# Kernel optimization log

Hardware: AMD Instinct MI355X
Metric: run time of the kernel (lower is better)

## Reference

```python
import jax, jax.numpy as jnp
import numpy as np

NUM_SEQS = 64
NUM_HEADS = 32
NUM_KV_HEADS = 8
HEAD_SIZE = 128
BLOCK_SIZE = 16
X = 8  # key cache vector width (16 bytes / fp16 elem size in vLLM)
NUM_BLOCKS = 4096
MAX_BLOCKS_PER_SEQ = 64
MAX_CTX = MAX_BLOCKS_PER_SEQ * BLOCK_SIZE  # 1024
SCALE = 0.08838834764831845  # 1/sqrt(HEAD_SIZE)
Q_PER_KV = NUM_HEADS // NUM_KV_HEADS


def setup_inputs() -> dict:
    key = jax.random.key(0)
    k0, k1, k2, k3, k4 = jax.random.split(key, 5)
    query = jax.random.normal(k0, (NUM_SEQS, NUM_HEADS, HEAD_SIZE), dtype=jnp.float32)
    key_cache = jax.random.normal(
        k1, (NUM_BLOCKS, NUM_KV_HEADS, HEAD_SIZE // X, BLOCK_SIZE, X), dtype=jnp.float32)
    value_cache = jax.random.normal(
        k2, (NUM_BLOCKS, NUM_KV_HEADS, HEAD_SIZE, BLOCK_SIZE), dtype=jnp.float32)
    block_tables = jax.random.randint(
        k3, (NUM_SEQS, MAX_BLOCKS_PER_SEQ), 0, NUM_BLOCKS, dtype=jnp.int32)
    context_lens = jax.random.randint(k4, (NUM_SEQS,), 1, MAX_CTX + 1, dtype=jnp.int32)
    return {"query": query, "key_cache": key_cache, "value_cache": value_cache,
            "block_tables": block_tables, "context_lens": context_lens}


def _paged_attention(query, key_cache, value_cache, block_tables, context_lens):
    nb = key_cache.shape[0]
    # key cache [nb, kvH, hs//x, bs, x] -> [nb, kvH, bs, hs]
    k_tok = jnp.transpose(key_cache, (0, 1, 3, 2, 4)).reshape(nb, NUM_KV_HEADS, BLOCK_SIZE, HEAD_SIZE)
    # value cache [nb, kvH, hs, bs] -> [nb, kvH, bs, hs]
    v_tok = jnp.transpose(value_cache, (0, 1, 3, 2))
    # gather per-sequence paged KV via block tables: [S, MB, kvH, bs, hs] -> [S, MAX_CTX, kvH, hs]
    keys = k_tok[block_tables].transpose(0, 1, 3, 2, 4).reshape(NUM_SEQS, MAX_CTX, NUM_KV_HEADS, HEAD_SIZE)
    values = v_tok[block_tables].transpose(0, 1, 3, 2, 4).reshape(NUM_SEQS, MAX_CTX, NUM_KV_HEADS, HEAD_SIZE)
    # GQA: group query heads over kv heads. q4: [S, kvH, qpkv, hs]
    q4 = query.reshape(NUM_SEQS, NUM_KV_HEADS, Q_PER_KV, HEAD_SIZE)
    # scores: [S, kvH, qpkv, MAX_CTX]
    scores = jnp.einsum('sgqd,skgd->sgqk', q4, keys) * SCALE
    valid = jnp.arange(MAX_CTX, dtype=jnp.int32)[None, :] < context_lens[:, None]  # [S, K]
    scores = jnp.where(valid[:, None, None, :], scores, jnp.float32(-1e30))
    probs = jax.nn.softmax(scores, axis=-1)
    out = jnp.einsum('sgqk,skgd->sgqd', probs, values)
    return out.reshape(NUM_SEQS, NUM_HEADS, HEAD_SIZE)


def reference(query, key_cache, value_cache, block_tables, context_lens):
    return _paged_attention(query, key_cache, value_cache, block_tables, context_lens)
```

## Files before the change

kernel.cpp:

```cpp
#include <hip/hip_runtime.h>

#define NSEQ   64
#define NHEAD  32
#define KVH    8
#define HS     128
#define BS     16
#define MBPS   64
#define MAXCTX 1024
#define QPKV   4
#define SCALE_F 0.08838834764831845f

__launch_bounds__(256)
__global__ void pa_kernel(const float* __restrict__ q,
                          const float* __restrict__ kc,
                          const float* __restrict__ vc,
                          const int*   __restrict__ bt,
                          const int*   __restrict__ cl,
                          float*       __restrict__ out)
{
    const int seq = blockIdx.x >> 3;
    const int kvh = blockIdx.x & 7;
    const int t   = threadIdx.x;
    const int ctx = cl[seq];
    const int nb  = (ctx + BS - 1) / BS;

    __shared__ __align__(16) float sc[QPKV][MAXCTX + 8];
    __shared__ float qs[QPKV][HS];
    __shared__ float l_inv[QPKV];

    for (int i = t; i < QPKV * HS; i += 256) {
        int g = i >> 7, d = i & 127;
        qs[g][d] = q[((size_t)seq * NHEAD + kvh * QPKV + g) * HS + d];
    }
    __syncthreads();

    const int tok   = t >> 4;
    const int dpart = t & 15;
    float qreg[QPKV][8];
#pragma unroll
    for (int g = 0; g < QPKV; ++g)
#pragma unroll
        for (int j = 0; j < 8; ++j)
            qreg[g][j] = qs[g][dpart * 8 + j];

    const int* btrow = bt + seq * MBPS;
    for (int b = 0; b < nb; ++b) {
        const int blk = btrow[b];
        const float* kptr = kc + ((size_t)blk * KVH + kvh) * (HS * BS)
                               + dpart * (BS * 8) + tok * 8;
        const float4 k0 = *(const float4*)kptr;
        const float4 k1 = *(const float4*)(kptr + 4);
        const float kk[8] = {k0.x,k0.y,k0.z,k0.w,k1.x,k1.y,k1.z,k1.w};
        float p[QPKV];
#pragma unroll
        for (int g = 0; g < QPKV; ++g) {
            float s = 0.f;
#pragma unroll
            for (int j = 0; j < 8; ++j) s += qreg[g][j] * kk[j];
            p[g] = s;
        }
#pragma unroll
        for (int off = 8; off >= 1; off >>= 1)
#pragma unroll
            for (int g = 0; g < QPKV; ++g)
                p[g] += __shfl_xor(p[g], off, 16);
        if (dpart < QPKV)
            sc[dpart][b * BS + tok] = p[dpart] * SCALE_F;
    }
    __syncthreads();

    {
        const int w    = t >> 6;
        const int lane = t & 63;
        float m = -1e30f;
        for (int i = lane; i < ctx; i += 64) m = fmaxf(m, sc[w][i]);
#pragma unroll
        for (int off = 32; off >= 1; off >>= 1) m = fmaxf(m, __shfl_xor(m, off));
        float ssum = 0.f;
        const int lim = nb * BS;
        for (int i = lane; i < lim; i += 64) {
            float v = (i < ctx) ? __expf(sc[w][i] - m) : 0.f;
            sc[w][i] = v;
            ssum += v;
        }
#pragma unroll
        for (int off = 32; off >= 1; off >>= 1) ssum += __shfl_xor(ssum, off);
        if (lane == 0) l_inv[w] = 1.f / ssum;
    }
    __syncthreads();

    const int d  = t >> 1;
    const int th = t & 1;
    float acc[QPKV] = {0.f, 0.f, 0.f, 0.f};
    for (int b = 0; b < nb; ++b) {
        const int blk = btrow[b];
        const float* vptr = vc + ((size_t)blk * KVH + kvh) * (HS * BS)
                               + d * BS + th * 8;
        const float4 v0 = *(const float4*)vptr;
        const float4 v1 = *(const float4*)(vptr + 4);
        const float vv[8] = {v0.x,v0.y,v0.z,v0.w,v1.x,v1.y,v1.z,v1.w};
        const int base = b * BS + th * 8;
#pragma unroll
        for (int g = 0; g < QPKV; ++g) {
            const float4 p0 = *(const float4*)&sc[g][base];
            const float4 p1 = *(const float4*)&sc[g][base + 4];
            acc[g] += p0.x*vv[0] + p0.y*vv[1] + p0.z*vv[2] + p0.w*vv[3]
                    + p1.x*vv[4] + p1.y*vv[5] + p1.z*vv[6] + p1.w*vv[7];
        }
    }
#pragma unroll
    for (int g = 0; g < QPKV; ++g)
        acc[g] += __shfl_xor(acc[g], 1);
    if (th == 0) {
#pragma unroll
        for (int g = 0; g < QPKV; ++g)
            out[((size_t)seq * NHEAD + kvh * QPKV + g) * HS + d] = acc[g] * l_inv[g];
    }
}

extern "C" void kernel_launch(void* const* d_in, const int* in_sizes, int n_in,
                              void* d_out, int out_size, void* d_ws, size_t ws_size,
                              hipStream_t stream) {
    const float* query       = (const float*)d_in[0];
    const float* key_cache   = (const float*)d_in[1];
    const float* value_cache = (const float*)d_in[2];
    const int*   block_tables= (const int*)d_in[3];
    const int*   context_lens= (const int*)d_in[4];
    float* out = (float*)d_out;

    dim3 grid(NSEQ * KVH);
    dim3 block(256);
    pa_kernel<<<grid, block, 0, stream>>>(query, key_cache, value_cache,
                                          block_tables, context_lens, out);
}
```

Baseline: 479.2 us.

## Split paged attention over context partitions with a separate combine kernel

Splits each sequence's context into 8 partitions of 128 tokens, one workgroup per partition, and each wave handles one query head of the group. Partial outputs, maxima and sums go to workspace, and a second kernel merges them with a log-sum-exp rescale. The aim is to raise parallelism beyond 512 workgroups and shorten the serial loop over blocks. In exchange it adds a second launch and workspace traffic, and each partition now loads K/V once per query head rather than once for all four.

```diff
diff --git a/kernel.cpp b/kernel.cpp
--- a/kernel.cpp
+++ b/kernel.cpp
@@ -6,130 +6,152 @@
 #define HS     128
 #define BS     16
 #define MBPS   64
-#define MAXCTX 1024
+#define PARTS  8
+#define PSIZE  128
 #define QPKV   4
 #define SCALE_F 0.08838834764831845f
 
-__launch_bounds__(256)
-__global__ void pa_kernel(const float* __restrict__ q,
-                          const float* __restrict__ kc,
-                          const float* __restrict__ vc,
-                          const int*   __restrict__ bt,
-                          const int*   __restrict__ cl,
-                          float*       __restrict__ out)
+#define O_PART_ELEMS (NSEQ*KVH*PARTS*QPKV*HS)
+#define ML_ELEMS     (NSEQ*KVH*PARTS*QPKV)
+
+__launch_bounds__(256, 4)
+__global__ void pa_part(const float* __restrict__ q,
+                        const float* __restrict__ kc,
+                        const float* __restrict__ vc,
+                        const int*   __restrict__ bt,
+                        const int*   __restrict__ cl,
+                        float*       __restrict__ o_part,
+                        float*       __restrict__ m_part,
+                        float*       __restrict__ l_part)
 {
-    const int seq = blockIdx.x >> 3;
-    const int kvh = blockIdx.x & 7;
-    const int t   = threadIdx.x;
-    const int ctx = cl[seq];
-    const int nb  = (ctx + BS - 1) / BS;
+    const int bx   = blockIdx.x;
+    const int part = bx & (PARTS - 1);
+    const int kvh  = (bx >> 3) & (KVH - 1);
+    const int seq  = bx >> 6;
+    const int ctx  = cl[seq];
+    const int tok0 = part * PSIZE;
+    if (tok0 >= ctx) return;
+    const int ntok = min(PSIZE, ctx - tok0);
+    const int nbl  = (ntok + BS - 1) / BS;
 
-    __shared__ __align__(16) float sc[QPKV][MAXCTX + 8];
-    __shared__ float qs[QPKV][HS];
-    __shared__ float l_inv[QPKV];
+    const int w    = threadIdx.x >> 6;
+    const int lane = threadIdx.x & 63;
+    const int tok  = lane & 15;
+    const int dq   = lane >> 4;
 
-    for (int i = t; i < QPKV * HS; i += 256) {
-        int g = i >> 7, d = i & 127;
-        qs[g][d] = q[((size_t)seq * NHEAD + kvh * QPKV + g) * HS + d];
+    __shared__ float sc[QPKV][PSIZE];
+
+    const float* qp = q + ((size_t)seq * NHEAD + kvh * QPKV + w) * HS + dq * 32;
+    float4 qv[8];
+#pragma unroll
+    for (int k = 0; k < 8; ++k) qv[k] = ((const float4*)qp)[k];
+
+    const int* btrow = bt + seq * MBPS + part * (PSIZE / BS);
+
+    for (int b = 0; b < nbl; ++b) {
+        const int blk = btrow[b];
+        const float* kb = kc + ((size_t)blk * KVH + kvh) * (HS * BS);
+        float s = 0.f;
+#pragma unroll
+        for (int k = 0; k < 4; ++k) {
+            const float4* kp = (const float4*)(kb + (dq * 4 + k) * (BS * 8) + tok * 8);
+            const float4 k0 = kp[0], k1 = kp[1];
+            const float4 q0 = qv[2 * k], q1 = qv[2 * k + 1];
+            s += q0.x*k0.x + q0.y*k0.y + q0.z*k0.z + q0.w*k0.w
+               + q1.x*k1.x + q1.y*k1.y + q1.z*k1.z + q1.w*k1.w;
+        }
+        s += __shfl_xor(s, 16);
+        s += __shfl_xor(s, 32);
+        if (lane < 16)
+            sc[w][b * BS + tok] = s * SCALE_F;
     }
-    __syncthreads();
 
-    const int tok   = t >> 4;
-    const int dpart = t & 15;
-    float qreg[QPKV][8];
+    float m = -1e30f;
+    for (int i = lane; i < ntok; i += 64) m = fmaxf(m, sc[w][i]);
 #pragma unroll
-    for (int g = 0; g < QPKV; ++g)
-#pragma unroll
-        for (int j = 0; j < 8; ++j)
-            qreg[g][j] = qs[g][dpart * 8 + j];
-
-    const int* btrow = bt + seq * MBPS;
-    for (int b = 0; b < nb; ++b) {
-        const int blk = btrow[b];
-        const float* kptr = kc + ((size_t)blk * KVH + kvh) * (HS * BS)
-                               + dpart * (BS * 8) + tok * 8;
-        const float4 k0 = *(const float4*)kptr;
-        const float4 k1 = *(const float4*)(kptr + 4);
-        const float kk[8] = {k0.x,k0.y,k0.z,k0.w,k1.x,k1.y,k1.z,k1.w};
-        float p[QPKV];
-#pragma unroll
-        for (int g = 0; g < QPKV; ++g) {
-            float s = 0.f;
-#pragma unroll
-            for (int j = 0; j < 8; ++j) s += qreg[g][j] * kk[j];
-            p[g] = s;
-        }
-#pragma unroll
-        for (int off = 8; off >= 1; off >>= 1)
-#pragma unroll
-            for (int g = 0; g < QPKV; ++g)
-                p[g] += __shfl_xor(p[g], off, 16);
-        if (dpart < QPKV)
-            sc[dpart][b * BS + tok] = p[dpart] * SCALE_F;
-    }
-    __syncthreads();
-
-    {
-        const int w    = t >> 6;
-        const int lane = t & 63;
-        float m = -1e30f;
-        for (int i = lane; i < ctx; i += 64) m = fmaxf(m, sc[w][i]);
-#pragma unroll
-        for (int off = 32; off >= 1; off >>= 1) m = fmaxf(m, __shfl_xor(m, off));
-        float ssum = 0.f;
-        const int lim = nb * BS;
-        for (int i = lane; i < lim; i += 64) {
-            float v = (i < ctx) ? __expf(sc[w][i] - m) : 0.f;
-            sc[w][i] = v;
-            ssum += v;
-        }
-#pragma unroll
-        for (int off = 32; off >= 1; off >>= 1) ssum += __shfl_xor(ssum, off);
-        if (lane == 0) l_inv[w] = 1.f / ssum;
-    }
-    __syncthreads();
-
-    const int d  = t >> 1;
-    const int th = t & 1;
-    float acc[QPKV] = {0.f, 0.f, 0.f, 0.f};
-    for (int b = 0; b < nb; ++b) {
-        const int blk = btrow[b];
-        const float* vptr = vc + ((size_t)blk * KVH + kvh) * (HS * BS)
-                               + d * BS + th * 8;
-        const float4 v0 = *(const float4*)vptr;
-        const float4 v1 = *(const float4*)(vptr + 4);
-        const float vv[8] = {v0.x,v0.y,v0.z,v0.w,v1.x,v1.y,v1.z,v1.w};
-        const int base = b * BS + th * 8;
-#pragma unroll
-        for (int g = 0; g < QPKV; ++g) {
-            const float4 p0 = *(const float4*)&sc[g][base];
-            const float4 p1 = *(const float4*)&sc[g][base + 4];
-            acc[g] += p0.x*vv[0] + p0.y*vv[1] + p0.z*vv[2] + p0.w*vv[3]
-                    + p1.x*vv[4] + p1.y*vv[5] + p1.z*vv[6] + p1.w*vv[7];
-        }
+    for (int off = 32; off >= 1; off >>= 1) m = fmaxf(m, __shfl_xor(m, off));
+    float lsum = 0.f;
+    const int lim = nbl * BS;
+    for (int i = lane; i < lim; i += 64) {
+        float v = (i < ntok) ? __expf(sc[w][i] - m) : 0.f;
+        sc[w][i] = v;
+        lsum += v;
     }
 #pragma unroll
-    for (int g = 0; g < QPKV; ++g)
-        acc[g] += __shfl_xor(acc[g], 1);
-    if (th == 0) {
-#pragma unroll
-        for (int g = 0; g < QPKV; ++g)
-            out[((size_t)seq * NHEAD + kvh * QPKV + g) * HS + d] = acc[g] * l_inv[g];
+    for (int off = 32; off >= 1; off >>= 1) lsum += __shfl_xor(lsum, off);
+
+    float acc0 = 0.f, acc1 = 0.f;
+    for (int b = 0; b < nbl; ++b) {
+        const int blk = btrow[b];
+        const float4* vp = (const float4*)(vc + ((size_t)blk * KVH + kvh) * (HS * BS)
+                                              + (size_t)lane * 32);
+        const float4 p0 = *(const float4*)&sc[w][b * BS + 0];
+        const float4 p1 = *(const float4*)&sc[w][b * BS + 4];
+        const float4 p2 = *(const float4*)&sc[w][b * BS + 8];
+        const float4 p3 = *(const float4*)&sc[w][b * BS + 12];
+        const float4 a0 = vp[0], a1 = vp[1], a2 = vp[2], a3 = vp[3];
+        const float4 b0 = vp[4], b1 = vp[5], b2 = vp[6], b3 = vp[7];
+        acc0 += p0.x*a0.x + p0.y*a0.y + p0.z*a0.z + p0.w*a0.w
+              + p1.x*a1.x + p1.y*a1.y + p1.z*a1.z + p1.w*a1.w
+              + p2.x*a2.x + p2.y*a2.y + p2.z*a2.z + p2.w*a2.w
+              + p3.x*a3.x + p3.y*a3.y + p3.z*a3.z + p3.w*a3.w;
+        acc1 += p0.x*b0.x + p0.y*b0.y + p0.z*b0.z + p0.w*b0.w
+              + p1.x*b1.x + p1.y*b1.y + p1.z*b1.z + p1.w*b1.w
+              + p2.x*b2.x + p2.y*b2.y + p2.z*b2.z + p2.w*b2.w
+              + p3.x*b3.x + p3.y*b3.y + p3.z*b3.z + p3.w*b3.w;
     }
+
+    const int    idx   = ((seq * KVH + kvh) * PARTS + part) * QPKV + w;
+    const size_t obase = (size_t)idx * HS;
+    ((float2*)(o_part + obase))[lane] = make_float2(acc0, acc1);
+    if (lane == 0) { m_part[idx] = m; l_part[idx] = lsum; }
+}
+
+__launch_bounds__(128)
+__global__ void pa_combine(const float* __restrict__ o_part,
+                           const float* __restrict__ m_part,
+                           const float* __restrict__ l_part,
+                           const int*   __restrict__ cl,
+                           float*       __restrict__ out)
+{
+    const int h   = blockIdx.x & (NHEAD - 1);
+    const int seq = blockIdx.x >> 5;
+    const int kvh = h >> 2;
+    const int g   = h & 3;
+    const int d   = threadIdx.x;
+    const int ctx = cl[seq];
+    const int np  = (ctx + PSIZE - 1) / PSIZE;
+
+    const int base = (seq * KVH + kvh) * PARTS * QPKV + g;
+    float M = -1e30f;
+    for (int p = 0; p < np; ++p)
+        M = fmaxf(M, m_part[base + p * QPKV]);
+    float L = 0.f, acc = 0.f;
+    for (int p = 0; p < np; ++p) {
+        const float w  = __expf(m_part[base + p * QPKV] - M);
+        L   += l_part[base + p * QPKV] * w;
+        acc += w * o_part[(size_t)(base + p * QPKV) * HS + d];
+    }
+    out[((size_t)seq * NHEAD + h) * HS + d] = acc / L;
 }
 
 extern "C" void kernel_launch(void* const* d_in, const int* in_sizes, int n_in,
                               void* d_out, int out_size, void* d_ws, size_t ws_size,
                               hipStream_t stream) {
-    const float* query       = (const float*)d_in[0];
-    const float* key_cache   = (const float*)d_in[1];
-    const float* value_cache = (const float*)d_in[2];
-    const int*   block_tables= (const int*)d_in[3];
-    const int*   context_lens= (const int*)d_in[4];
+    const float* query        = (const float*)d_in[0];
+    const float* key_cache    = (const float*)d_in[1];
+    const float* value_cache  = (const float*)d_in[2];
+    const int*   block_tables = (const int*)d_in[3];
+    const int*   context_lens = (const int*)d_in[4];
     float* out = (float*)d_out;
 
-    dim3 grid(NSEQ * KVH);
-    dim3 block(256);
-    pa_kernel<<<grid, block, 0, stream>>>(query, key_cache, value_cache,
-                                          block_tables, context_lens, out);
+    float* o_part = (float*)d_ws;
+    float* m_part = o_part + O_PART_ELEMS;
+    float* l_part = m_part + ML_ELEMS;
+
+    pa_part<<<dim3(NSEQ * KVH * PARTS), dim3(256), 0, stream>>>(
+        query, key_cache, value_cache, block_tables, context_lens,
+        o_part, m_part, l_part);
+    pa_combine<<<dim3(NSEQ * NHEAD), dim3(128), 0, stream>>>(
+        o_part, m_part, l_part, context_lens, out);
 }
```

After: 587.4 us. 1.23x slower.
